# Kernel tuning notes

Measured on AMD Instinct MI355X. Metric: run time of the kernel, lower is better.

The kernel has to match this reference:

```python
import jax, jax.numpy as jnp
import numpy as np

B, NP, C_IN, H = 8, 6250, 512, 256   # graphs, nodes/graph, in-feat, hidden
EPG = 100000                          # edges per graph
K = 5000                              # ceil(0.8 * NP) kept by TopKPooling
H3 = 3 * H


def setup_inputs() -> dict:
    key = jax.random.key(0)
    ks = jax.random.split(key, 16)
    N, E = B * NP, B * EPG
    x = jax.random.normal(ks[0], (N, C_IN), jnp.float32)
    offs = (jnp.arange(E) // EPG) * NP  # keep edges inside their graph
    src = jax.random.randint(ks[1], (E,), 0, NP) + offs
    dst = jax.random.randint(ks[2], (E,), 0, NP) + offs
    edge_index = jnp.stack([src, dst]).astype(jnp.int64)
    edge_attr = jax.random.uniform(ks[3], (E,), jnp.float32)
    batch = jnp.repeat(jnp.arange(B), NP).astype(jnp.int64)
    s = 0.05
    W1 = jax.random.normal(ks[4], (C_IN, H), jnp.float32) * s
    b1 = jnp.zeros((H,), jnp.float32)
    W2 = jax.random.normal(ks[5], (H, H), jnp.float32) * s
    b2 = jnp.zeros((H,), jnp.float32)
    pw = jax.random.normal(ks[6], (H3,), jnp.float32) * s   # TopKPooling attn vector
    lw1 = jax.random.normal(ks[7], (H3 * 2, H), jnp.float32) * s
    lb1 = jnp.zeros((H,), jnp.float32)
    lw2 = jax.random.normal(ks[8], (H, H // 2), jnp.float32) * s
    lb2 = jnp.zeros((H // 2,), jnp.float32)
    lw3 = jax.random.normal(ks[9], (H // 2, 3), jnp.float32) * s
    lb3 = jnp.zeros((3,), jnp.float32)
    return {"x": x, "edge_index": edge_index, "edge_attr": edge_attr, "batch": batch,
            "W1": W1, "b1": b1, "W2": W2, "b2": b2, "pw": pw,
            "lw1": lw1, "lb1": lb1, "lw2": lw2, "lb2": lb2, "lw3": lw3, "lb3": lb3}


def _gcn(x, W, b, src, dst, ew, n):
    xw = x @ W
    deg = jnp.zeros((n,), xw.dtype).at[dst].add(ew) + 1.0
    dinv = jax.lax.rsqrt(deg)
    norm = dinv[src] * ew * dinv[dst]
    out = jnp.zeros_like(xw).at[dst].add(norm[:, None] * xw[src])
    return out + (dinv * dinv)[:, None] * xw + b


def reference(x, edge_index, edge_attr, batch, W1, b1, W2, b2, pw,
              lw1, lb1, lw2, lb2, lw3, lb3):
    N = x.shape[0]
    src, dst = edge_index[0], edge_index[1]
    x1 = jax.nn.relu(_gcn(x, W1, b1, src, dst, edge_attr, N))
    x2 = jax.nn.relu(_gcn(x1, W2, b2, src, dst, edge_attr, N))
    x3 = jax.nn.relu(_gcn(x2, W2, b2, src, dst, edge_attr, N))  # conv2 reused (as in source)
    cat_x = jnp.concatenate([x1, x2, x3], axis=1)               # [N, 3H]
    # TopKPooling: score = sigmoid((x . w) / ||w||), keep top-K per graph, scale by score
    score = jax.nn.sigmoid((cat_x @ pw) / jnp.linalg.norm(pw))   # [N]
    sc = score.reshape(B, NP)
    topv, topi = jax.lax.top_k(sc, K)                            # [B, K]
    xg = cat_x.reshape(B, NP, H3)
    sel = jnp.take_along_axis(xg, topi[:, :, None], axis=1) * topv[:, :, None]  # [B, K, 3H]
    readout = jnp.concatenate([sel.mean(axis=1), sel.max(axis=1)], axis=1)      # [B, 6H]
    h = jax.nn.relu(readout @ lw1 + lb1)
    h = jax.nn.relu(h @ lw2 + lb2)       # dropout p=0 is a no-op
    return h @ lw3 + lb3                 # [B, 3]
```

## Files before the change

### kernel.cpp

```cpp
#include <hip/hip_runtime.h>
#include <stdint.h>

#define NODES  50000
#define MPAD   50048
#define NGRAPH 8
#define NP_G   6250
#define EPG    100000
#define EDGES  800000
#define KKEEP  5000
#define HID    256
#define CIN    512
#define H3     768
#define SCANB  196
#define RCHUNK 200
#define MLPCH  24
#define MLPCK  64
#define ESL    3125

#define K1_HIST  512
#define K1_CAST  25000
#define K1_W1    512
#define K1_W2    256
#define K1_TOTAL (K1_HIST + K1_CAST + K1_W1 + K1_W2 + 1)
#define K2_GEMM  782
#define K2_FILL  256
#define K2_TOTAL (K2_GEMM + K2_FILL)

using f32x4  = __attribute__((ext_vector_type(4))) float;
using bf16x8 = __attribute__((ext_vector_type(8))) short;
using u16x8  = __attribute__((ext_vector_type(8))) unsigned short;
typedef unsigned short u16;
typedef unsigned int   u32;
typedef unsigned long long u64;

__device__ __forceinline__ float bf2f(u16 u) {
    return __uint_as_float(((uint32_t)u) << 16);
}
__device__ __forceinline__ u16 f2bf(float f) {
    uint32_t u = __float_as_uint(f);
    u += 0x7fffu + ((u >> 16) & 1u);
    return (u16)(u >> 16);
}

__global__ __launch_bounds__(256) void k1_kernel(
        const int* __restrict__ ei, const float* __restrict__ ew,
        u64* __restrict__ partial,
        const float* __restrict__ x, u16* __restrict__ A0,
        const float* __restrict__ W1, const float* __restrict__ W2,
        const float* __restrict__ pw,
        u16* __restrict__ Wt1, u16* __restrict__ Wt2, float* __restrict__ invn) {
    __shared__ __align__(16) char smem[ESL * 8];
    int b = blockIdx.x, t = threadIdx.x;
    if (b < K1_HIST) {
        u64* hl = (u64*)smem;
        int g  = b >> 6;
        int r  = b & 63;
        int bb = r >> 1;
        int h  = r & 1;
        for (int k = t; k < ESL; k += 256) hl[k] = 0ull;
        __syncthreads();
        int ebase = g * EPG + bb * ESL;
        int lo = h * ESL;
        for (int k = t; k < ESL; k += 256) {
            int e = ebase + k;
            int d = ei[EDGES + e];
            int il = d - g * NP_G - lo;
            if ((unsigned)il < (unsigned)ESL) {
                u64 enc = (1ull << 48) | (u64)(ew[e] * 4294967296.0f);
                atomicAdd(&hl[il], enc);
            }
        }
        __syncthreads();
        u64* prow = partial + (size_t)(g * 32 + bb) * NP_G + lo;
        for (int k = t; k < ESL; k += 256) prow[k] = hl[k];
    } else if (b < K1_HIST + K1_CAST) {
        size_t base = ((size_t)(b - K1_HIST) * 256 + t) * 4;
        float4 v = *(const float4*)(x + base);
        ushort4 o;
        o.x = f2bf(v.x); o.y = f2bf(v.y); o.z = f2bf(v.z); o.w = f2bf(v.w);
        *(ushort4*)(A0 + base) = o;
    } else if (b < K1_HIST + K1_CAST + K1_W1) {
        int id = (b - K1_HIST - K1_CAST) * 256 + t;
        int n = id >> 9, k = id & 511;
        Wt1[id] = f2bf(W1[(size_t)k * HID + n]);
    } else if (b < K1_TOTAL - 1) {
        int id = (b - K1_HIST - K1_CAST - K1_W1) * 256 + t;
        int n = id >> 8, k = id & 255;
        Wt2[id] = f2bf(W2[(size_t)k * HID + n]);
    } else {
        float* sh = (float*)smem;
        float s = 0.f;
        for (int i = t; i < H3; i += 256) { float v = pw[i]; s += v * v; }
        sh[t] = s; __syncthreads();
        for (int off = 128; off; off >>= 1) {
            if (t < off) sh[t] += sh[t + off];
            __syncthreads();
        }
        if (t == 0) invn[0] = rsqrtf(sh[0]);
    }
}

__global__ void scan1_kernel(const u64* __restrict__ partial,
                             u32* __restrict__ blockbase,
                             int* __restrict__ iscan, int* __restrict__ bsum,
                             float* __restrict__ dinv) {
    int b = blockIdx.x, t = threadIdx.x;
    int i = b * 256 + t;
    int c = 0;
    if (i < NODES) {
        int g = i / NP_G, il = i - g * NP_G;
        size_t base = (size_t)(g * 32) * NP_G + il;
        u64 fix = 0ull; u32 cnt = 0;
#pragma unroll 4
        for (int j = 0; j < 32; ++j) {
            size_t idx = base + (size_t)j * NP_G;
            u64 pv = partial[idx];
            blockbase[idx] = cnt;
            cnt += (u32)(pv >> 48);
            fix += pv & 0xFFFFFFFFFFFFull;
        }
        c = (int)cnt;
        float deg = (float)fix * (1.0f / 4294967296.0f);
        dinv[i] = rsqrtf(deg + 1.0f);
    }
    int lane = t & 63, wv = t >> 6;
    int v = c;
    for (int off = 1; off < 64; off <<= 1) {
        int u = __shfl_up(v, off);
        if (lane >= off) v += u;
    }
    __shared__ int ws[4];
    if (lane == 63) ws[wv] = v;
    __syncthreads();
    if (t == 0) { int s = 0; for (int k = 0; k < 4; k++) { int tmp = ws[k]; ws[k] = s; s += tmp; } }
    __syncthreads();
    v += ws[wv];
    if (i < NODES) iscan[i] = v - c;
    if (t == 255) bsum[b] = v;
}

__global__ void scan2_kernel(const int* __restrict__ bsum, int* __restrict__ boff) {
    int t = threadIdx.x;
    int c = (t < SCANB) ? bsum[t] : 0;
    int lane = t & 63, wv = t >> 6;
    int v = c;
    for (int off = 1; off < 64; off <<= 1) {
        int u = __shfl_up(v, off);
        if (lane >= off) v += u;
    }
    __shared__ int ws[4];
    if (lane == 63) ws[wv] = v;
    __syncthreads();
    if (t == 0) { int s = 0; for (int k = 0; k < 4; k++) { int tmp = ws[k]; ws[k] = s; s += tmp; } }
    __syncthreads();
    v += ws[wv];
    if (t < SCANB) boff[t] = v - c;
}

__global__ void scan3_kernel(const int* __restrict__ iscan, const int* __restrict__ boff,
                             int* __restrict__ rowptr) {
    int b = blockIdx.x, t = threadIdx.x;
    int i = b * 256 + t;
    if (i > NODES) return;
    if (i == NODES) { rowptr[NODES] = EDGES; return; }
    rowptr[i] = boff[b] + iscan[i];
}

__device__ __forceinline__ void gemm_body(const u16* __restrict__ A,
                                          const u16* __restrict__ Bt,
                                          u16* __restrict__ C,
                                          int K, int bm, int bn,
                                          u16* As, u16* Bs) {
    const int tid  = threadIdx.x;
    const int wave = tid >> 6, lane = tid & 63;
    const int wm = wave >> 1, wn = wave & 1;
    const int quad = lane >> 4, l16 = lane & 15;
    const int sr = tid >> 2;
    const int sc = tid & 3;
    const int swz = (sc ^ ((sr >> 1) & 3)) * 8;
    const int rphys = (quad ^ ((l16 >> 1) & 3)) * 8;

    const u16* Ag = A + (size_t)(bm * 128 + sr) * K + sc * 8;
    const u16* Bg = Bt + (size_t)(bn * 128 + sr) * K + sc * 8;

    f32x4 acc[4][4];
#pragma unroll
    for (int i = 0; i < 4; i++)
#pragma unroll
        for (int j = 0; j < 4; j++) { f32x4 z = {0.f, 0.f, 0.f, 0.f}; acc[i][j] = z; }

    for (int k0 = 0; k0 < K; k0 += 32) {
        int4 av0 = *(const int4*)(Ag + k0);
        int4 av1 = *(const int4*)(Ag + (size_t)64 * K + k0);
        int4 bv0 = *(const int4*)(Bg + k0);
        int4 bv1 = *(const int4*)(Bg + (size_t)64 * K + k0);
        __syncthreads();
        *(int4*)(As + sr * 32 + swz)        = av0;
        *(int4*)(As + (sr + 64) * 32 + swz) = av1;
        *(int4*)(Bs + sr * 32 + swz)        = bv0;
        *(int4*)(Bs + (sr + 64) * 32 + swz) = bv1;
        __syncthreads();
        bf16x8 af[4], bfr[4];
#pragma unroll
        for (int i = 0; i < 4; i++)
            af[i] = *(const bf16x8*)(As + (wm * 64 + i * 16 + l16) * 32 + rphys);
#pragma unroll
        for (int j = 0; j < 4; j++)
            bfr[j] = *(const bf16x8*)(Bs + (wn * 64 + j * 16 + l16) * 32 + rphys);
#pragma unroll
        for (int i = 0; i < 4; i++)
#pragma unroll
            for (int j = 0; j < 4; j++)
                acc[i][j] = __builtin_amdgcn_mfma_f32_16x16x32_bf16(af[i], bfr[j], acc[i][j], 0, 0, 0);
    }

    const int crow0 = bm * 128 + wm * 64 + quad * 4;
    const int ccol0 = bn * 128 + wn * 64 + l16;
#pragma unroll
    for (int i = 0; i < 4; i++)
#pragma unroll
        for (int j = 0; j < 4; j++)
#pragma unroll
            for (int r = 0; r < 4; r++)
                C[(size_t)(crow0 + i * 16 + r) * HID + ccol0 + j * 16] = f2bf(acc[i][j][r]);
}

__global__ __launch_bounds__(256) void k2_kernel(
        const u16* __restrict__ A0, const u16* __restrict__ Wt1, u16* __restrict__ xw,
        const int* __restrict__ ei, const float* __restrict__ ew,
        const float* __restrict__ dinv, const int* __restrict__ rowptr,
        const u32* __restrict__ blockbase, int2* __restrict__ csr) {
    __shared__ __align__(16) char smem[NP_G * 4];
    int b = blockIdx.x;
    if (b < K2_GEMM) {
        u16* As = (u16*)smem;
        u16* Bs = (u16*)(smem + 8192);
        gemm_body(A0, Wt1, xw, CIN, b >> 1, b & 1, As, Bs);
    } else {
        u32* cursor = (u32*)smem;
        int g  = b & 7;
        int bb = (b - K2_GEMM) >> 3;
        const u32* bbase = blockbase + (size_t)(g * 32 + bb) * NP_G;
        const int* rp = rowptr + g * NP_G;
        for (int k = threadIdx.x; k < NP_G; k += 256)
            cursor[k] = (u32)rp[k] + bbase[k];
        __syncthreads();
        int ebase = g * EPG + bb * ESL;
#pragma unroll 4
        for (int k = threadIdx.x; k < ESL; k += 256) {
            int e = ebase + k;
            int s = ei[e], d = ei[EDGES + e];
            int il = d - g * NP_G;
            u32 pos = atomicAdd(&cursor[il], 1u);
            csr[pos] = make_int2(s, __float_as_int(dinv[s] * ew[e] * dinv[d]));
        }
    }
}

__global__ __launch_bounds__(256) void gemm_bt(const u16* __restrict__ A,
                                               const u16* __restrict__ Bt,
                                               u16* __restrict__ C, int K) {
    __shared__ u16 As[128 * 32];
    __shared__ u16 Bs[128 * 32];
    gemm_body(A, Bt, C, K, blockIdx.x, blockIdx.y, As, Bs);
}

template<bool SCORE>
__global__ void agg_kernel(const u16* __restrict__ xw, u16* __restrict__ xo,
                           const int* __restrict__ rowptr, const int2* __restrict__ csr,
                           const float* __restrict__ dinv, const float* __restrict__ bias,
                           const u16* __restrict__ xs1, const u16* __restrict__ xs2,
                           const float* __restrict__ pw, const float* __restrict__ invn,
                           float* __restrict__ score, u64* __restrict__ keys) {
    int wave = threadIdx.x >> 6;
    int lane = threadIdx.x & 63;
    int g  = blockIdx.x & 7;
    int nl = (blockIdx.x >> 3) * 4 + wave;
    if (nl >= NP_G) return;
    int w = g * NP_G + nl;
    int half = lane >> 5;
    int f8 = (lane & 31) * 8;
    size_t ro = (size_t)w * HID + f8;

    float accA[8], accB[8];
#pragma unroll
    for (int j = 0; j < 8; ++j) { accA[j] = 0.f; accB[j] = 0.f; }

    int p = rowptr[w], p1 = rowptr[w + 1];
    for (; p + 4 <= p1; p += 4) {
        int2 eA = csr[p + half];
        int2 eB = csr[p + 2 + half];
        float wA = __int_as_float(eA.y), wB = __int_as_float(eB.y);
        u16x8 vA = *(const u16x8*)(xw + (size_t)eA.x * HID + f8);
        u16x8 vB = *(const u16x8*)(xw + (size_t)eB.x * HID + f8);
#pragma unroll
        for (int j = 0; j < 8; ++j) {
            accA[j] += wA * bf2f(vA[j]);
            accB[j] += wB * bf2f(vB[j]);
        }
    }
    for (; p < p1; p += 2) {
        int idx = p + half;
        bool valid = idx < p1;
        int2 eA = csr[valid ? idx : p];
        float wA = valid ? __int_as_float(eA.y) : 0.f;
        u16x8 vA = *(const u16x8*)(xw + (size_t)eA.x * HID + f8);
#pragma unroll
        for (int j = 0; j < 8; ++j) accA[j] += wA * bf2f(vA[j]);
    }

#pragma unroll
    for (int j = 0; j < 8; ++j) {
        accA[j] += accB[j];
        accA[j] += __shfl(accA[j], lane ^ 32, 64);
    }

    float di = dinv[w], sw = di * di;
    u16x8 sv = *(const u16x8*)(xw + ro);
    float bb[8];
    {
        float4 t0 = *(const float4*)(bias + f8);
        float4 t1 = *(const float4*)(bias + f8 + 4);
        bb[0] = t0.x; bb[1] = t0.y; bb[2] = t0.z; bb[3] = t0.w;
        bb[4] = t1.x; bb[5] = t1.y; bb[6] = t1.z; bb[7] = t1.w;
    }
    u16x8 o;
    float ov[8];
#pragma unroll
    for (int j = 0; j < 8; ++j) {
        float v = fmaxf(accA[j] + sw * bf2f(sv[j]) + bb[j], 0.f);
        o[j] = f2bf(v);
        ov[j] = bf2f(o[j]);
    }
    if (half == 0) *(u16x8*)(xo + ro) = o;

    if (SCORE) {
        u16x8 v1 = *(const u16x8*)(xs1 + ro);
        u16x8 v2 = *(const u16x8*)(xs2 + ro);
        float acc = 0.f;
#pragma unroll
        for (int j = 0; j < 8; ++j) {
            acc += bf2f(v1[j]) * pw[f8 + j];
            acc += bf2f(v2[j]) * pw[256 + f8 + j];
            acc += ov[j]       * pw[512 + f8 + j];
        }
#pragma unroll
        for (int off = 1; off < 32; off <<= 1) acc += __shfl_xor(acc, off, 64);
        if (lane == 0) {
            float s = acc * invn[0];
            float sc = 1.f / (1.f + __expf(-s));
            score[w] = sc;
            keys[w] = ((u64)__float_as_uint(sc) << 13) | (unsigned int)(NP_G - 1 - nl);
        }
    }
}

__global__ __launch_bounds__(1024) void selcomp_kernel(
        const u64* __restrict__ keys, const float* __restrict__ score,
        int* __restrict__ selidx, float* __restrict__ selscr) {
    __shared__ u64 kk[NP_G];
    __shared__ unsigned int hist[4][256];
    __shared__ unsigned int sfx[257];
    __shared__ u64 spref;
    __shared__ unsigned int swant;
    int g = blockIdx.x, t = threadIdx.x;
    const u64* kg = keys + (size_t)g * NP_G;
    for (int i = t; i < NP_G; i += 1024) kk[i] = kg[i];
    if (t == 0) { spref = 0ull; swant = KKEEP; }
    const int wgrp = (t >> 8) & 3;
    u64 mask = 0ull;
    __syncthreads();
    for (int shift = 40; shift >= 0; shift -= 8) {
        if (t < 256) { hist[0][t] = 0; hist[1][t] = 0; hist[2][t] = 0; hist[3][t] = 0; }
        __syncthreads();
        u64 pref = spref;
        for (int i = t; i < NP_G; i += 1024) {
            u64 key = kk[i];
            if ((key & mask) == pref)
                atomicAdd(&hist[wgrp][(unsigned int)(key >> shift) & 255u], 1u);
        }
        __syncthreads();
        if (t < 256) sfx[t] = hist[0][t] + hist[1][t] + hist[2][t] + hist[3][t];
        if (t == 0) sfx[256] = 0;
        __syncthreads();
        for (int off = 1; off < 256; off <<= 1) {
            unsigned int v = 0;
            if (t < 256 && t + off < 256) v = sfx[t + off];
            __syncthreads();
            if (t < 256 && t + off < 256) sfx[t] += v;
            __syncthreads();
        }
        unsigned int want = swant;
        __syncthreads();
        if (t < 256) {
            unsigned int s0 = sfx[t], s1 = sfx[t + 1];
            if (s0 >= want && s1 < want) {
                spref = pref | ((u64)t << shift);
                swant = want - s1;
            }
        }
        __syncthreads();
        mask |= (255ull << shift);
    }
    u64 kth = spref;
    int lane = t & 63, wv = t >> 6;
    __shared__ int wsum[16];
    __shared__ int cbase;
    if (t == 0) cbase = 0;
    __syncthreads();
    for (int k = 0; k < (NP_G + 1023) / 1024; ++k) {
        int i = k * 1024 + t;
        bool sel = (i < NP_G) && (kk[i] >= kth);
        int n = g * NP_G + i;
        u64 bal = __ballot(sel);
        int prefix = __popcll(bal & ((1ull << lane) - 1ull));
        if (lane == 0) wsum[wv] = __popcll(bal);
        __syncthreads();
        if (t == 0) {
            int s = cbase;
            for (int j = 0; j < 16; ++j) { int tmp = wsum[j]; wsum[j] = s; s += tmp; }
            cbase = s;
        }
        __syncthreads();
        if (sel) {
            int pos = wsum[wv] + prefix;
            selidx[g * KKEEP + pos] = n;
            selscr[g * KKEEP + pos] = score[n];
        }
        __syncthreads();
    }
}

__global__ __launch_bounds__(256) void readout_kernel(
        const u16* __restrict__ x1, const u16* __restrict__ x2,
        const u16* __restrict__ x3,
        const int* __restrict__ selidx, const float* __restrict__ selscr,
        float* __restrict__ sumbuf, int* __restrict__ maxbuf) {
    int g = blockIdx.x, tpart = blockIdx.y, c = blockIdx.z;
    int fcol = threadIdx.x;
    const u16* xt = (tpart == 0) ? x1 : ((tpart == 1) ? x2 : x3);
    __shared__ int   sidx[RCHUNK];
    __shared__ float sscr[RCHUNK];
    int base = g * KKEEP + c * RCHUNK;
    if (fcol < RCHUNK) { sidx[fcol] = selidx[base + fcol]; sscr[fcol] = selscr[base + fcol]; }
    __syncthreads();
    float sum = 0.f, mx = 0.f;
#pragma unroll 1
    for (int j = 0; j < RCHUNK; j += 4) {
        int n0 = sidx[j], n1 = sidx[j + 1], n2 = sidx[j + 2], n3 = sidx[j + 3];
        float s0 = sscr[j], s1 = sscr[j + 1], s2 = sscr[j + 2], s3 = sscr[j + 3];
        float v0 = bf2f(xt[(size_t)n0 * HID + fcol]) * s0;
        float v1 = bf2f(xt[(size_t)n1 * HID + fcol]) * s1;
        float v2 = bf2f(xt[(size_t)n2 * HID + fcol]) * s2;
        float v3 = bf2f(xt[(size_t)n3 * HID + fcol]) * s3;
        sum += v0 + v1 + v2 + v3;
        mx = fmaxf(mx, fmaxf(fmaxf(v0, v1), fmaxf(v2, v3)));
    }
    int o = (g * 3 + tpart) * HID + fcol;
    atomicAdd(&sumbuf[o], sum);
    atomicMax(&maxbuf[o], __float_as_int(mx));
}

__global__ __launch_bounds__(256) void mlp1_kernel(const float* __restrict__ sumbuf,
                                                   const int* __restrict__ maxbuf,
                                                   const float* __restrict__ lw1,
                                                   float* __restrict__ h1acc) {
    int g = blockIdx.x, ch = blockIdx.y, t = threadIdx.x;
    __shared__ float r[MLPCK];
    int k0 = ch * MLPCK;
    if (t < MLPCK) {
        int i = k0 + t;
        r[t] = (i < 768) ? sumbuf[g * 768 + i] * (1.f / 5000.f)
                         : __int_as_float(maxbuf[g * 768 + (i - 768)]);
    }
    __syncthreads();
    float a0 = 0.f, a1 = 0.f, a2 = 0.f, a3 = 0.f;
#pragma unroll
    for (int i = 0; i < MLPCK; i += 4) {
        a0 += r[i]     * lw1[(size_t)(k0 + i)     * 256 + t];
        a1 += r[i + 1] * lw1[(size_t)(k0 + i + 1) * 256 + t];
        a2 += r[i + 2] * lw1[(size_t)(k0 + i + 2) * 256 + t];
        a3 += r[i + 3] * lw1[(size_t)(k0 + i + 3) * 256 + t];
    }
    atomicAdd(&h1acc[g * 256 + t], (a0 + a1) + (a2 + a3));
}

__global__ __launch_bounds__(256) void mlp2_kernel(const float* __restrict__ h1acc,
                                                   const float* __restrict__ lb1,
                                                   const float* __restrict__ lw2,
                                                   const float* __restrict__ lb2,
                                                   const float* __restrict__ lw3,
                                                   const float* __restrict__ lb3,
                                                   float* __restrict__ out) {
    __shared__ float h1[256];
    __shared__ float part[256];
    __shared__ float h2[128];
    int g = blockIdx.x, t = threadIdx.x;
    h1[t] = fmaxf(h1acc[g * 256 + t] + lb1[t], 0.f);
    __syncthreads();
    int col = t & 127, half = t >> 7;
    float a = 0.f;
#pragma unroll
    for (int i = 0; i < 128; i += 4) {
        int k = half * 128 + i;
        a += h1[k]     * lw2[k * 128 + col]
           + h1[k + 1] * lw2[(k + 1) * 128 + col]
           + h1[k + 2] * lw2[(k + 2) * 128 + col]
           + h1[k + 3] * lw2[(k + 3) * 128 + col];
    }
    part[t] = a;
    __syncthreads();
    if (t < 128) h2[t] = fmaxf(part[t] + part[t + 128] + lb2[t], 0.f);
    __syncthreads();
    if (t < 3) {
        float a3 = lb3[t];
        for (int i = 0; i < 128; ++i) a3 += h2[i] * lw3[i * 3 + t];
        out[g * 3 + t] = a3;
    }
}

extern "C" void kernel_launch(void* const* d_in, const int* in_sizes, int n_in,
                              void* d_out, int out_size, void* d_ws, size_t ws_size,
                              hipStream_t stream) {
    const float* x   = (const float*)d_in[0];
    const int*   ei  = (const int*)d_in[1];
    const float* ew  = (const float*)d_in[2];
    const float* W1  = (const float*)d_in[4];
    const float* b1  = (const float*)d_in[5];
    const float* W2  = (const float*)d_in[6];
    const float* b2  = (const float*)d_in[7];
    const float* pw  = (const float*)d_in[8];
    const float* lw1 = (const float*)d_in[9];
    const float* lb1 = (const float*)d_in[10];
    const float* lw2 = (const float*)d_in[11];
    const float* lb2 = (const float*)d_in[12];
    const float* lw3 = (const float*)d_in[13];
    const float* lb3 = (const float*)d_in[14];
    float* out = (float*)d_out;

    char* p = (char*)d_ws;
    auto alloc = [&](size_t bytes) -> char* {
        char* r = p;
        p += (bytes + 255) & ~(size_t)255;
        return r;
    };
    u16* A0  = (u16*)alloc((size_t)MPAD * CIN * 2);
    u16* x3  = (u16*)alloc((size_t)MPAD * HID * 2);
    u16* xw  = (u16*)alloc((size_t)MPAD * HID * 2);
    u16* Wt1 = (u16*)alloc((size_t)HID * CIN * 2);
    u16* Wt2 = (u16*)alloc((size_t)HID * HID * 2);
    int2*  csr    = (int2*)alloc((size_t)EDGES * 8);
    u64*   partial   = (u64*)alloc((size_t)256 * NP_G * 8);
    u32*   blockbase = (u32*)alloc((size_t)256 * NP_G * 4);
    int*   rowptr = (int*)alloc((size_t)(NODES + 1) * 4);
    int*   iscan  = (int*)alloc((size_t)NODES * 4);
    int*   bsum   = (int*)alloc((size_t)SCANB * 4);
    int*   boff   = (int*)alloc((size_t)SCANB * 4);
    u64*   keys   = (u64*)alloc((size_t)NODES * 8);
    float* score  = (float*)alloc((size_t)NODES * 4);
    float* dinv   = (float*)alloc((size_t)NODES * 4);
    int*   selidx = (int*)alloc((size_t)NGRAPH * KKEEP * 4);
    float* selscr = (float*)alloc((size_t)NGRAPH * KKEEP * 4);
    float* invn   = (float*)alloc(256);
    char* zbase = p;
    float* sumbuf = (float*)alloc(6144 * 4);
    int*   maxbuf = (int*)alloc(6144 * 4);
    float* h1acc  = (float*)alloc((size_t)NGRAPH * 256 * 4);
    size_t zbytes = (size_t)(p - zbase);

    u16* x1 = A0;
    u16* x2 = A0 + (size_t)MPAD * HID;

    hipMemsetAsync(zbase, 0, zbytes, stream);

    k1_kernel<<<K1_TOTAL, 256, 0, stream>>>(ei, ew, partial, x, A0,
                                            W1, W2, pw, Wt1, Wt2, invn);
    scan1_kernel<<<SCANB, 256, 0, stream>>>(partial, blockbase, iscan, bsum, dinv);
    scan2_kernel<<<1, 256, 0, stream>>>(bsum, boff);
    scan3_kernel<<<SCANB + 1, 256, 0, stream>>>(iscan, boff, rowptr);
    k2_kernel<<<K2_TOTAL, 256, 0, stream>>>(A0, Wt1, xw, ei, ew, dinv, rowptr,
                                            blockbase, csr);

    dim3 gg(MPAD / 128, HID / 128);
    int aggBlocks = 8 * ((NP_G + 3) / 4);

    agg_kernel<false><<<aggBlocks, 256, 0, stream>>>(xw, x1, rowptr, csr, dinv, b1,
                                                     nullptr, nullptr, nullptr, nullptr,
                                                     nullptr, nullptr);
    gemm_bt<<<gg, 256, 0, stream>>>(x1, Wt2, xw, HID);
    agg_kernel<false><<<aggBlocks, 256, 0, stream>>>(xw, x2, rowptr, csr, dinv, b2,
                                                     nullptr, nullptr, nullptr, nullptr,
                                                     nullptr, nullptr);
    gemm_bt<<<gg, 256, 0, stream>>>(x2, Wt2, xw, HID);
    agg_kernel<true><<<aggBlocks, 256, 0, stream>>>(xw, x3, rowptr, csr, dinv, b2,
                                                    x1, x2, pw, invn, score, keys);

    selcomp_kernel<<<NGRAPH, 1024, 0, stream>>>(keys, score, selidx, selscr);
    readout_kernel<<<dim3(NGRAPH, 3, KKEEP / RCHUNK), 256, 0, stream>>>(
        x1, x2, x3, selidx, selscr, sumbuf, maxbuf);
    mlp1_kernel<<<dim3(NGRAPH, MLPCH), 256, 0, stream>>>(sumbuf, maxbuf, lw1, h1acc);
    mlp2_kernel<<<NGRAPH, 256, 0, stream>>>(h1acc, lb1, lw2, lb2, lw3, lb3, out);
}
```

Measured before the change: 479.6 us.

## Remap GEMM tiles to XCDs and batch CSR edge loads via wave shuffles

GEMM blocks are now remapped so consecutive row tiles land on the same XCD (blockIdx mod 8), keeping A-tile and output locality within one XCD's L2; a 784-block grid with early-exit padding is used for both GEMM launches. The aggregation kernel now loads up to 64 CSR entries per wave in one coalesced read and broadcasts source/weight via shuffles, unrolling 8 edges per iteration to increase memory-level parallelism. This adds shuffle overhead and wasted tail lanes for low-degree nodes.

Result: faster. 462.8 us (-3.5%).

```diff
diff --git a/kernel.cpp b/kernel.cpp
--- a/kernel.cpp
+++ b/kernel.cpp
@@ -22,7 +22,8 @@
 #define K1_W1    512
 #define K1_W2    256
 #define K1_TOTAL (K1_HIST + K1_CAST + K1_W1 + K1_W2 + 1)
-#define K2_GEMM  782
+#define GEMM_GRID 784
+#define K2_GEMM  GEMM_GRID
 #define K2_FILL  256
 #define K2_TOTAL (K2_GEMM + K2_FILL)
 
@@ -166,6 +167,15 @@
     rowptr[i] = boff[b] + iscan[i];
 }
 
+__device__ __forceinline__ bool gemm_map(int i, int& bm, int& bn) {
+    int g = i & 7, s = i >> 3;
+    int cnt = (g == 5) ? 48 : 49;
+    if ((s >> 1) >= cnt) return false;
+    bm = 49 * g - (g > 5 ? 1 : 0) + (s >> 1);
+    bn = s & 1;
+    return true;
+}
+
 __device__ __forceinline__ void gemm_body(const u16* __restrict__ A,
                                           const u16* __restrict__ Bt,
                                           u16* __restrict__ C,
@@ -233,9 +243,11 @@
     __shared__ __align__(16) char smem[NP_G * 4];
     int b = blockIdx.x;
     if (b < K2_GEMM) {
+        int bm, bn;
+        if (!gemm_map(b, bm, bn)) return;
         u16* As = (u16*)smem;
         u16* Bs = (u16*)(smem + 8192);
-        gemm_body(A0, Wt1, xw, CIN, b >> 1, b & 1, As, Bs);
+        gemm_body(A0, Wt1, xw, CIN, bm, bn, As, Bs);
     } else {
         u32* cursor = (u32*)smem;
         int g  = b & 7;
@@ -262,7 +274,9 @@
                                                u16* __restrict__ C, int K) {
     __shared__ u16 As[128 * 32];
     __shared__ u16 Bs[128 * 32];
-    gemm_body(A, Bt, C, K, blockIdx.x, blockIdx.y, As, Bs);
+    int bm, bn;
+    if (!gemm_map(blockIdx.x, bm, bn)) return;
+    gemm_body(A, Bt, C, K, bm, bn, As, Bs);
 }
 
 template<bool SCORE>
@@ -282,37 +296,55 @@
     int f8 = (lane & 31) * 8;
     size_t ro = (size_t)w * HID + f8;
 
-    float accA[8], accB[8];
-#pragma unroll
-    for (int j = 0; j < 8; ++j) { accA[j] = 0.f; accB[j] = 0.f; }
+    float acc0[8], acc1[8];
+#pragma unroll
+    for (int j = 0; j < 8; ++j) { acc0[j] = 0.f; acc1[j] = 0.f; }
 
     int p = rowptr[w], p1 = rowptr[w + 1];
-    for (; p + 4 <= p1; p += 4) {
-        int2 eA = csr[p + half];
-        int2 eB = csr[p + 2 + half];
-        float wA = __int_as_float(eA.y), wB = __int_as_float(eB.y);
-        u16x8 vA = *(const u16x8*)(xw + (size_t)eA.x * HID + f8);
-        u16x8 vB = *(const u16x8*)(xw + (size_t)eB.x * HID + f8);
-#pragma unroll
-        for (int j = 0; j < 8; ++j) {
-            accA[j] += wA * bf2f(vA[j]);
-            accB[j] += wB * bf2f(vB[j]);
-        }
-    }
-    for (; p < p1; p += 2) {
-        int idx = p + half;
-        bool valid = idx < p1;
-        int2 eA = csr[valid ? idx : p];
-        float wA = valid ? __int_as_float(eA.y) : 0.f;
-        u16x8 vA = *(const u16x8*)(xw + (size_t)eA.x * HID + f8);
-#pragma unroll
-        for (int j = 0; j < 8; ++j) accA[j] += wA * bf2f(vA[j]);
+    for (int q = p; q < p1; q += 64) {
+        int m = min(64, p1 - q);
+        int2 e = make_int2(0, 0);
+        if (lane < m) e = csr[q + lane];
+        int j = 0;
+        for (; j + 8 <= m; j += 8) {
+            int i0 = j + half,     i1 = j + 2 + half;
+            int i2 = j + 4 + half, i3 = j + 6 + half;
+            int   s0 = __shfl(e.x, i0, 64); float w0 = __int_as_float(__shfl(e.y, i0, 64));
+            int   s1 = __shfl(e.x, i1, 64); float w1 = __int_as_float(__shfl(e.y, i1, 64));
+            int   s2 = __shfl(e.x, i2, 64); float w2 = __int_as_float(__shfl(e.y, i2, 64));
+            int   s3 = __shfl(e.x, i3, 64); float w3 = __int_as_float(__shfl(e.y, i3, 64));
+            u16x8 v0 = *(const u16x8*)(xw + (size_t)s0 * HID + f8);
+            u16x8 v1 = *(const u16x8*)(xw + (size_t)s1 * HID + f8);
+            u16x8 v2 = *(const u16x8*)(xw + (size_t)s2 * HID + f8);
+            u16x8 v3 = *(const u16x8*)(xw + (size_t)s3 * HID + f8);
+#pragma unroll
+            for (int t = 0; t < 8; ++t) {
+                acc0[t] += w0 * bf2f(v0[t]);
+                acc1[t] += w1 * bf2f(v1[t]);
+                acc0[t] += w2 * bf2f(v2[t]);
+                acc1[t] += w3 * bf2f(v3[t]);
+            }
+        }
+        for (; j + 2 <= m; j += 2) {
+            int i0 = j + half;
+            int s0 = __shfl(e.x, i0, 64); float w0 = __int_as_float(__shfl(e.y, i0, 64));
+            u16x8 v0 = *(const u16x8*)(xw + (size_t)s0 * HID + f8);
+#pragma unroll
+            for (int t = 0; t < 8; ++t) acc0[t] += w0 * bf2f(v0[t]);
+        }
+        if (j < m) {
+            int s0 = __shfl(e.x, j, 64); float w0 = __int_as_float(__shfl(e.y, j, 64));
+            w0 = half ? 0.f : w0;
+            u16x8 v0 = *(const u16x8*)(xw + (size_t)s0 * HID + f8);
+#pragma unroll
+            for (int t = 0; t < 8; ++t) acc0[t] += w0 * bf2f(v0[t]);
+        }
     }
 
 #pragma unroll
     for (int j = 0; j < 8; ++j) {
-        accA[j] += accB[j];
-        accA[j] += __shfl(accA[j], lane ^ 32, 64);
+        acc0[j] += acc1[j];
+        acc0[j] += __shfl(acc0[j], lane ^ 32, 64);
     }
 
     float di = dinv[w], sw = di * di;
@@ -328,7 +360,7 @@
     float ov[8];
 #pragma unroll
     for (int j = 0; j < 8; ++j) {
-        float v = fmaxf(accA[j] + sw * bf2f(sv[j]) + bb[j], 0.f);
+        float v = fmaxf(acc0[j] + sw * bf2f(sv[j]) + bb[j], 0.f);
         o[j] = f2bf(v);
         ov[j] = bf2f(o[j]);
     }
@@ -581,17 +613,16 @@
     k2_kernel<<<K2_TOTAL, 256, 0, stream>>>(A0, Wt1, xw, ei, ew, dinv, rowptr,
                                             blockbase, csr);
 
-    dim3 gg(MPAD / 128, HID / 128);
     int aggBlocks = 8 * ((NP_G + 3) / 4);
 
     agg_kernel<false><<<aggBlocks, 256, 0, stream>>>(xw, x1, rowptr, csr, dinv, b1,
                                                      nullptr, nullptr, nullptr, nullptr,
                                                      nullptr, nullptr);
-    gemm_bt<<<gg, 256, 0, stream>>>(x1, Wt2, xw, HID);
+    gemm_bt<<<GEMM_GRID, 256, 0, stream>>>(x1, Wt2, xw, HID);
     agg_kernel<false><<<aggBlocks, 256, 0, stream>>>(xw, x2, rowptr, csr, dinv, b2,
                                                      nullptr, nullptr, nullptr, nullptr,
                                                      nullptr, nullptr);
-    gemm_bt<<<gg, 256, 0, stream>>>(x2, Wt2, xw, HID);
+    gemm_bt<<<GEMM_GRID, 256, 0, stream>>>(x2, Wt2, xw, HID);
     agg_kernel<true><<<aggBlocks, 256, 0, stream>>>(xw, x3, rowptr, csr, dinv, b2,
                                                     x1, x2, pw, invn, score, keys);
 
```
